# Kernel tuning notes

Hardware: AMD Instinct MI355X
Metric: run time of the kernel (lower is better)

The kernel has to match this reference:

```python
import jax, jax.numpy as jnp
import numpy as np
import math

D_MODEL = 1024
N_HEADS = 16
BATCH = 2
SEQ = 2048

def setup_inputs() -> dict:
    key = jax.random.key(0)
    ks = jax.random.split(key, 5)
    d = D_MODEL
    lim_qkv = 1.0 / math.sqrt(d)
    x = jax.random.normal(ks[0], (BATCH, SEQ, d), dtype=jnp.float32)
    qkv_w = jax.random.uniform(ks[1], (3 * d, d), dtype=jnp.float32, minval=-lim_qkv, maxval=lim_qkv)
    qkv_b = jax.random.uniform(ks[2], (3 * d,), dtype=jnp.float32, minval=-lim_qkv, maxval=lim_qkv)
    out_w = jax.random.uniform(ks[3], (d, d), dtype=jnp.float32, minval=-lim_qkv, maxval=lim_qkv)
    out_b = jax.random.uniform(ks[4], (d,), dtype=jnp.float32, minval=-lim_qkv, maxval=lim_qkv)
    return {"x": x, "qkv_w": qkv_w, "qkv_b": qkv_b, "out_w": out_w, "out_b": out_b}

def reference(x, qkv_w, qkv_b, out_w, out_b):
    b, s, d = x.shape
    h = N_HEADS
    hd = d // h
    # note: original uses float division for scale: sqrt(in_features / n_heads)
    scale = math.sqrt(d / h)
    qkv = x @ qkv_w.T + qkv_b                      # [b, s, 3d]
    q, k, v = jnp.split(qkv, 3, axis=-1)           # each [b, s, d]
    def heads(t):
        return t.reshape(b, s, h, hd).transpose(0, 2, 1, 3)  # [b, h, s, hd]
    qh, kh, vh = heads(q), heads(k), heads(v)
    # faithful quirk: scores = k @ q^T (k as query, q as key)
    scores = jnp.einsum('bhid,bhjd->bhij', kh, qh) / scale   # [b, h, s, s]
    alpha = jax.nn.softmax(scores, axis=-1)
    attn = jnp.einsum('bhij,bhjd->bhid', alpha, vh)          # [b, h, s, hd]
    attn = attn.transpose(0, 2, 1, 3).reshape(b, s, d)       # [b, s, d]
    return attn @ out_w.T + out_b
```

## Files before the change

kernel.cpp:

```cpp
#include <hip/hip_runtime.h>
#include <hip/hip_fp16.h>

#define D_MODEL 1024
#define N_HEADS 16
#define HEAD_DIM 64
#define BATCH 2
#define SEQ 2048
#define ROWS (BATCH*SEQ)

#define K_SCALE 0.18033688011112042f

using h8v = __attribute__((ext_vector_type(8))) _Float16;
using h4v = __attribute__((ext_vector_type(4))) _Float16;
using g2v = __attribute__((ext_vector_type(2))) __fp16;
using g4v = __attribute__((ext_vector_type(4))) __fp16;
using f4v = __attribute__((ext_vector_type(4))) float;

__device__ __forceinline__ ushort f2h_u(float x) { return __half_as_ushort(__float2half(x)); }
__device__ __forceinline__ void splith(float x, ushort& h, ushort& l) {
    __half hh_ = __float2half(x);
    h = __half_as_ushort(hh_);
    l = f2h_u(x - __half2float(hh_));
}

__device__ __forceinline__ size_t fidx(int row, int k) {
    return ((size_t)((row >> 7) * 32 + (k >> 5)) << 12)
         + (size_t)(((row & 127) >> 4) << 9)
         + (size_t)(((row & 15) * 4 + ((k & 31) >> 3)) << 3) + (k & 7);
}

__device__ __forceinline__ void async_lds16(const ushort* g, ushort* l) {
    __builtin_amdgcn_global_load_lds(
        (const __attribute__((address_space(1))) unsigned int*)g,
        (__attribute__((address_space(3))) unsigned int*)l, 16, 0, 0);
}

__global__ __launch_bounds__(256)
void prep_kernel(const float* __restrict__ x, const float* __restrict__ qw,
                 const float* __restrict__ ow,
                 ushort* __restrict__ xh, ushort* __restrict__ qwh,
                 ushort* __restrict__ owh, ushort* __restrict__ owl)
{
    const int b = blockIdx.x, t = threadIdx.x;
    if (b < 4096) {
        const int i = b * 256 + t;
        const int row = i >> 8, k4 = (i & 255) * 4;
        const float4 v = ((const float4*)x)[i];
        ushort4 h;
        h.x = f2h_u(v.x); h.y = f2h_u(v.y); h.z = f2h_u(v.z); h.w = f2h_u(v.w);
        *(ushort4*)&xh[fidx(row, k4)] = h;
    } else if (b < 7168) {
        const int i = (b - 4096) * 256 + t;
        const int row = i >> 8, k4 = (i & 255) * 4;
        const float4 v = ((const float4*)qw)[i];
        ushort4 h;
        h.x = f2h_u(v.x); h.y = f2h_u(v.y); h.z = f2h_u(v.z); h.w = f2h_u(v.w);
        *(ushort4*)&qwh[fidx(row, k4)] = h;
    } else {
        const int i = (b - 7168) * 256 + t;
        const int row = i >> 8, k4 = (i & 255) * 4;
        const float4 v = ((const float4*)ow)[i];
        const size_t o = fidx(row, k4);
        ushort4 h, l;
        splith(v.x, h.x, l.x); splith(v.y, h.y, l.y);
        splith(v.z, h.z, l.z); splith(v.w, h.w, l.w);
        *(ushort4*)&owh[o] = h; *(ushort4*)&owl[o] = l;
    }
}

__global__ __launch_bounds__(256, 5)
void gemm_qkv(const ushort* __restrict__ Af, const ushort* __restrict__ Wf,
              const float* __restrict__ bias,
              ushort* __restrict__ Qh, ushort* __restrict__ Kh,
              ushort* __restrict__ Vt)
{
    __shared__ ushort sA[2][4096], sW[2][2048];
    const int t = threadIdx.x, lane = t & 63, wv = t >> 6;
    const int tx = lane & 15, g = lane >> 4;
    const int lin = blockIdx.x;
    const int xcd = lin & 7, r = lin >> 3;
    const int mb = xcd * 4 + (r & 3);
    const int nb = r >> 2;
    const int at0 = (wv >> 1) * 4, wt0 = (wv & 1) * 2;
    const int fo = (tx * 4 + g) * 8;
    const size_t wbase = ((size_t)(nb & 1)) << 11;

    f4v acc[8];
#pragma unroll
    for (int i = 0; i < 8; i++)
#pragma unroll
        for (int e = 0; e < 4; e++) acc[i][e] = 0.f;

    {
        const size_t ao = ((size_t)(mb * 32)) << 12;
        const size_t wo = (((size_t)((nb >> 1) * 32)) << 12) + wbase;
#pragma unroll
        for (int c = 0; c < 2; c++) {
            const int o = (t + c * 256) * 8;
            async_lds16(Af + ao + o, &sA[0][o]);
        }
        async_lds16(Wf + wo + t * 8, &sW[0][t * 8]);
    }

    for (int kt = 0; kt < 32; kt++) {
        const int p = kt & 1;
        __syncthreads();
        if (kt < 31) {
            const size_t ao = ((size_t)(mb * 32 + kt + 1)) << 12;
            const size_t wo = (((size_t)((nb >> 1) * 32 + kt + 1)) << 12) + wbase;
#pragma unroll
            for (int c = 0; c < 2; c++) {
                const int o = (t + c * 256) * 8;
                async_lds16(Af + ao + o, &sA[p ^ 1][o]);
            }
            async_lds16(Wf + wo + t * 8, &sW[p ^ 1][t * 8]);
        }
        h8v ah[4], wh[2];
#pragma unroll
        for (int i = 0; i < 4; i++)
            ah[i] = *(const h8v*)&sA[p][(at0 + i) * 512 + fo];
#pragma unroll
        for (int i = 0; i < 2; i++)
            wh[i] = *(const h8v*)&sW[p][(wt0 + i) * 512 + fo];
        if (nb < 32) {
#pragma unroll
            for (int wi = 0; wi < 2; wi++)
#pragma unroll
                for (int ai = 0; ai < 4; ai++)
                    acc[wi * 4 + ai] = __builtin_amdgcn_mfma_f32_16x16x32_f16(wh[wi], ah[ai], acc[wi * 4 + ai], 0, 0, 0);
        } else {
#pragma unroll
            for (int ai = 0; ai < 4; ai++)
#pragma unroll
                for (int wi = 0; wi < 2; wi++)
                    acc[ai * 2 + wi] = __builtin_amdgcn_mfma_f32_16x16x32_f16(ah[ai], wh[wi], acc[ai * 2 + wi], 0, 0, 0);
        }
    }

    if (nb < 32) {
        const int part = nb >> 4;
        ushort* dst = part ? Kh : Qh;
        const float scale = part ? K_SCALE : 1.0f;
#pragma unroll
        for (int wi = 0; wi < 2; wi++) {
            const int gf0 = nb * 64 + (wv & 1) * 32 + wi * 16 + g * 4;
            const float4 bv = *(const float4*)&bias[gf0];
            const int gfl = gf0 & 1023;
            const int hh = gfl >> 6;
            const int dd = gfl & 63;
#pragma unroll
            for (int ai = 0; ai < 4; ai++) {
                const int s = mb * 128 + (wv >> 1) * 64 + ai * 16 + tx;
                const int bb = s >> 11, srel = s & 2047;
                const size_t idx = (size_t)(bb * N_HEADS + hh) * 131072
                    + (size_t)(srel >> 4) * 1024 + (size_t)(dd >> 5) * 512
                    + ((srel & 15) * 4 + ((dd & 31) >> 3)) * 8 + (dd & 7);
                const f4v a = acc[wi * 4 + ai];
                ushort4 h4;
                h4.x = f2h_u((a[0] + bv.x) * scale);
                h4.y = f2h_u((a[1] + bv.y) * scale);
                h4.z = f2h_u((a[2] + bv.z) * scale);
                h4.w = f2h_u((a[3] + bv.w) * scale);
                *(ushort4*)&dst[idx] = h4;
            }
        }
    } else {
#pragma unroll
        for (int wi = 0; wi < 2; wi++) {
            const int gf = nb * 64 + (wv & 1) * 32 + wi * 16 + tx;
            const float bv = bias[gf];
            const int gfl = gf & 1023;
            const int hh = gfl >> 6;
            const int dl = gfl & 63;
#pragma unroll
            for (int ai = 0; ai < 4; ai++) {
                const int jt0 = mb * 128 + (wv >> 1) * 64 + ai * 16 + g * 4;
                const int bb = jt0 >> 11, jr = jt0 & 2047;
                const size_t idx = (size_t)(bb * N_HEADS + hh) * 131072
                    + (size_t)(jr >> 6) * 4096
                    + (size_t)((((jr >> 4) & 3) * 4) + (dl >> 4)) * 256
                    + (((jr >> 2) & 3) * 16 + (dl & 15)) * 4;
                const f4v a = acc[ai * 2 + wi];
                ushort4 h4;
                h4.x = f2h_u(a[0] + bv);
                h4.y = f2h_u(a[1] + bv);
                h4.z = f2h_u(a[2] + bv);
                h4.w = f2h_u(a[3] + bv);
                *(ushort4*)&Vt[idx] = h4;
            }
        }
    }
}

__global__ __launch_bounds__(256)
void attn_mfma(const ushort* __restrict__ Kf, const ushort* __restrict__ Qf,
               const ushort* __restrict__ Vf,
               ushort* __restrict__ Oh, ushort* __restrict__ Ol)
{
    __shared__ ushort lds[16384];
    ushort* K0 = lds + 8192;

    const int t = threadIdx.x, lane = t & 63, wv = t >> 6;
    const int tx = lane & 15, g = lane >> 4;
    const int lin = blockIdx.x;
    const int xcd = lin & 7, ix = lin >> 3;
    const int bh = xcd * 4 + (ix >> 4);
    const int it = ix & 15;
    const int b = bh >> 4, h = bh & 15;
    const int i0 = it * 128;
    const size_t hb = (size_t)bh * 131072;

    {
        const size_t kb = hb + (size_t)it * 8192;
#pragma unroll
        for (int c = 0; c < 4; c++) {
            const int o = (t + c * 256) * 8;
            async_lds16(Kf + kb + o, K0 + o);
        }
#pragma unroll
        for (int c = 0; c < 2; c++) {
            const int o = (t + c * 256) * 8;
            async_lds16(Qf + hb + o, lds + o);
            async_lds16(Vf + hb + o, lds + 4096 + o);
        }
    }
    __syncthreads();

    const int fo = (tx * 4 + g) * 8;
    h8v kf[2][2];
#pragma unroll
    for (int is = 0; is < 2; is++)
#pragma unroll
        for (int kk = 0; kk < 2; kk++)
            kf[is][kk] = *(const h8v*)&K0[((wv * 2 + is) * 2 + kk) * 512 + fo];

    f4v O[2][4];
    float l_acc[2] = {0.f, 0.f};
#pragma unroll
    for (int is = 0; is < 2; is++)
#pragma unroll
        for (int ht = 0; ht < 4; ht++)
#pragma unroll
            for (int e = 0; e < 4; e++) O[is][ht][e] = 0.f;

    for (int jt = 0; jt < SEQ / 64; jt++) {
        ushort* buf = lds + (jt & 1) * 8192;
        ushort* nxt = lds + ((jt & 1) ^ 1) * 8192;
        __syncthreads();
        if (jt < SEQ / 64 - 1) {
            const size_t off = hb + (size_t)(jt + 1) * 4096;
#pragma unroll
            for (int c = 0; c < 2; c++) {
                const int o = (t + c * 256) * 8;
                async_lds16(Qf + off + o, nxt + o);
                async_lds16(Vf + off + o, nxt + 4096 + o);
            }
        }
        const ushort* sQ = buf;
        const ushort* sV = buf + 4096;

        f4v sc[2][4];
#pragma unroll
        for (int is = 0; is < 2; is++)
#pragma unroll
            for (int jn = 0; jn < 4; jn++)
#pragma unroll
                for (int e = 0; e < 4; e++) sc[is][jn][e] = 0.f;
#pragma unroll
        for (int kk = 0; kk < 2; kk++)
#pragma unroll
            for (int jn = 0; jn < 4; jn++) {
                const h8v qf = *(const h8v*)&sQ[(jn * 2 + kk) * 512 + fo];
#pragma unroll
                for (int is = 0; is < 2; is++)
                    sc[is][jn] = __builtin_amdgcn_mfma_f32_16x16x32_f16(qf, kf[is][kk], sc[is][jn], 0, 0, 0);
            }

        h4v ph[2][4];
#pragma unroll
        for (int is = 0; is < 2; is++)
#pragma unroll
            for (int jn = 0; jn < 4; jn++) {
                const float p0 = __builtin_amdgcn_exp2f(sc[is][jn][0]);
                const float p1 = __builtin_amdgcn_exp2f(sc[is][jn][1]);
                const float p2 = __builtin_amdgcn_exp2f(sc[is][jn][2]);
                const float p3 = __builtin_amdgcn_exp2f(sc[is][jn][3]);
                l_acc[is] += (p0 + p1) + (p2 + p3);
                const g2v plo = __builtin_amdgcn_cvt_pkrtz(p0, p1);
                const g2v phi = __builtin_amdgcn_cvt_pkrtz(p2, p3);
                const g4v pk = __builtin_shufflevector(plo, phi, 0, 1, 2, 3);
                ph[is][jn] = __builtin_bit_cast(h4v, pk);
            }

#pragma unroll
        for (int jc = 0; jc < 4; jc++)
#pragma unroll
            for (int ht = 0; ht < 4; ht++) {
                const h4v vf = *(const h4v*)&sV[(jc * 4 + ht) * 256 + (g * 16 + tx) * 4];
#pragma unroll
                for (int is = 0; is < 2; is++)
                    O[is][ht] = __builtin_amdgcn_mfma_f32_16x16x16f16(vf, ph[is][jc], O[is][ht], 0, 0, 0);
            }
    }

#pragma unroll
    for (int is = 0; is < 2; is++) {
        float l = l_acc[is];
        l += __shfl_xor(l, 16);
        l += __shfl_xor(l, 32);
        const float inv = 1.0f / l;
        const int row = b * SEQ + i0 + (wv * 2 + is) * 16 + tx;
#pragma unroll
        for (int ht = 0; ht < 4; ht++) {
            const int k0 = h * 64 + ht * 16 + g * 4;
            const size_t o = fidx(row, k0);
            ushort4 hv, lv;
            float v;
            v = O[is][ht][0] * inv; splith(v, hv.x, lv.x);
            v = O[is][ht][1] * inv; splith(v, hv.y, lv.y);
            v = O[is][ht][2] * inv; splith(v, hv.z, lv.z);
            v = O[is][ht][3] * inv; splith(v, hv.w, lv.w);
            *(ushort4*)&Oh[o] = hv;
            *(ushort4*)&Ol[o] = lv;
        }
    }
}

__global__ __launch_bounds__(256, 4)
void gemm_out(const ushort* __restrict__ Af, const ushort* __restrict__ Alf,
              const ushort* __restrict__ Wf, const ushort* __restrict__ Wlf,
              const float* __restrict__ bias, float* __restrict__ out)
{
    __shared__ ushort sA[2][4096], sW[2][4096];
    const int t = threadIdx.x, lane = t & 63, wv = t >> 6;
    const int tx = lane & 15, g = lane >> 4;
    const int lin = blockIdx.x;
    const int xcd = lin & 7, r = lin >> 3;
    const int nb = xcd * 2 + (r & 1);
    const int mb = r >> 1;
    const int at0 = (wv >> 1) * 2, wt0 = (wv & 1) * 2;
    const int fo = (tx * 4 + g) * 8;
    const size_t abase = ((size_t)(mb & 1)) << 11;
    const size_t wbase = ((size_t)(nb & 1)) << 11;

    f4v acc[4];
#pragma unroll
    for (int i = 0; i < 4; i++)
#pragma unroll
        for (int e = 0; e < 4; e++) acc[i][e] = 0.f;

    {
        const size_t ao = (((size_t)((mb >> 1) * 32)) << 12) + abase;
        const size_t wo = (((size_t)((nb >> 1) * 32)) << 12) + wbase;
        const int o = t * 8;
        async_lds16(Af + ao + o, &sA[0][o]);
        async_lds16(Alf + ao + o, &sA[0][2048 + o]);
        async_lds16(Wf + wo + o, &sW[0][o]);
        async_lds16(Wlf + wo + o, &sW[0][2048 + o]);
    }

    for (int kt = 0; kt < 32; kt++) {
        const int p = kt & 1;
        __syncthreads();
        if (kt < 31) {
            const size_t ao = (((size_t)((mb >> 1) * 32 + kt + 1)) << 12) + abase;
            const size_t wo = (((size_t)((nb >> 1) * 32 + kt + 1)) << 12) + wbase;
            const int o = t * 8;
            async_lds16(Af + ao + o, &sA[p ^ 1][o]);
            async_lds16(Alf + ao + o, &sA[p ^ 1][2048 + o]);
            async_lds16(Wf + wo + o, &sW[p ^ 1][o]);
            async_lds16(Wlf + wo + o, &sW[p ^ 1][2048 + o]);
        }
        h8v ah[2], al[2], wh[2], wl[2];
#pragma unroll
        for (int i = 0; i < 2; i++) {
            ah[i] = *(const h8v*)&sA[p][(at0 + i) * 512 + fo];
            al[i] = *(const h8v*)&sA[p][2048 + (at0 + i) * 512 + fo];
            wh[i] = *(const h8v*)&sW[p][(wt0 + i) * 512 + fo];
            wl[i] = *(const h8v*)&sW[p][2048 + (wt0 + i) * 512 + fo];
        }
#pragma unroll
        for (int wi = 0; wi < 2; wi++)
#pragma unroll
            for (int ai = 0; ai < 2; ai++) {
                acc[wi * 2 + ai] = __builtin_amdgcn_mfma_f32_16x16x32_f16(wh[wi], ah[ai], acc[wi * 2 + ai], 0, 0, 0);
                acc[wi * 2 + ai] = __builtin_amdgcn_mfma_f32_16x16x32_f16(wh[wi], al[ai], acc[wi * 2 + ai], 0, 0, 0);
                acc[wi * 2 + ai] = __builtin_amdgcn_mfma_f32_16x16x32_f16(wl[wi], ah[ai], acc[wi * 2 + ai], 0, 0, 0);
            }
    }

#pragma unroll
    for (int wi = 0; wi < 2; wi++) {
        const int gf0 = nb * 64 + (wv & 1) * 32 + wi * 16 + g * 4;
        const float4 bv = *(const float4*)&bias[gf0];
#pragma unroll
        for (int ai = 0; ai < 2; ai++) {
            const int tok = mb * 64 + (wv >> 1) * 32 + ai * 16 + tx;
            const f4v a = acc[wi * 2 + ai];
            float4 o;
            o.x = a[0] + bv.x;
            o.y = a[1] + bv.y;
            o.z = a[2] + bv.z;
            o.w = a[3] + bv.w;
            *(float4*)&out[(size_t)tok * D_MODEL + gf0] = o;
        }
    }
}

extern "C" void kernel_launch(void* const* d_in, const int* in_sizes, int n_in,
                              void* d_out, int out_size, void* d_ws, size_t ws_size,
                              hipStream_t stream) {
    const float* x     = (const float*)d_in[0];
    const float* qkv_w = (const float*)d_in[1];
    const float* qkv_b = (const float*)d_in[2];
    const float* out_w = (const float*)d_in[3];
    const float* out_b = (const float*)d_in[4];
    float* out = (float*)d_out;

    const size_t FB = (size_t)ROWS * D_MODEL;
    const size_t MM = (size_t)D_MODEL * D_MODEL;
    ushort* u   = (ushort*)d_ws;
    ushort* xh  = u;
    ushort* Ol  = u + FB;
    ushort* Qh  = u + 2 * FB;
    ushort* Kh  = u + 3 * FB;
    ushort* Vt  = u + 4 * FB;
    ushort* qwh = u + 5 * FB;
    ushort* owh = u + 5 * FB + 3 * MM;
    ushort* owl = owh + MM;

    prep_kernel<<<8192, 256, 0, stream>>>(x, qkv_w, out_w, xh, qwh, owh, owl);
    gemm_qkv<<<1536, 256, 0, stream>>>(xh, qwh, qkv_b, Qh, Kh, Vt);
    attn_mfma<<<512, 256, 0, stream>>>(Kh, Qh, Vt, xh, Ol);
    gemm_out<<<1024, 256, 0, stream>>>(xh, Ol, owh, owl, out_b, out);
}
```

Baseline: 215.4 us.

## Software-pipeline attention loop with triple buffering and 16x16x32 PV MFMA

Restructures the attention inner loop so the PV MFMAs for the previous tile run alongside the QK scores for the current tile, and the exp2 softmax step for the current tile comes after them. Q/V tiles are triple-buffered in a larger LDS allocation to make this possible. The V layout written by the QKV projection is also changed so PV can use 16x16x32 MFMA with 8-wide fragments, halving the number of PV MFMA instructions. The cost is more LDS per block (64KB), which may reduce occupancy, and extra live registers for the carried probabilities.

```diff
diff --git a/kernel.cpp b/kernel.cpp
--- a/kernel.cpp
+++ b/kernel.cpp
@@ -176,10 +176,14 @@
             for (int ai = 0; ai < 4; ai++) {
                 const int jt0 = mb * 128 + (wv >> 1) * 64 + ai * 16 + g * 4;
                 const int bb = jt0 >> 11, jr = jt0 & 2047;
+                const int jj = jr & 63;
                 const size_t idx = (size_t)(bb * N_HEADS + hh) * 131072
                     + (size_t)(jr >> 6) * 4096
-                    + (size_t)((((jr >> 4) & 3) * 4) + (dl >> 4)) * 256
-                    + (((jr >> 2) & 3) * 16 + (dl & 15)) * 4;
+                    + (size_t)(jj >> 5) * 2048
+                    + (size_t)((dl >> 4) & 3) * 512
+                    + (size_t)((jj >> 2) & 3) * 128
+                    + (size_t)(dl & 15) * 8
+                    + (size_t)((jj >> 4) & 1) * 4;
                 const f4v a = acc[ai * 2 + wi];
                 ushort4 h4;
                 h4.x = f2h_u(a[0] + bv);
@@ -197,8 +201,9 @@
                const ushort* __restrict__ Vf,
                ushort* __restrict__ Oh, ushort* __restrict__ Ol)
 {
-    __shared__ ushort lds[16384];
-    ushort* K0 = lds + 8192;
+    __shared__ ushort lds[32768];
+    ushort* KR = lds;
+    ushort* bufs = lds + 8192;
 
     const int t = threadIdx.x, lane = t & 63, wv = t >> 6;
     const int tx = lane & 15, g = lane >> 4;
@@ -215,24 +220,35 @@
 #pragma unroll
         for (int c = 0; c < 4; c++) {
             const int o = (t + c * 256) * 8;
-            async_lds16(Kf + kb + o, K0 + o);
+            async_lds16(Kf + kb + o, KR + o);
         }
 #pragma unroll
         for (int c = 0; c < 2; c++) {
             const int o = (t + c * 256) * 8;
-            async_lds16(Qf + hb + o, lds + o);
-            async_lds16(Vf + hb + o, lds + 4096 + o);
+            async_lds16(Qf + hb + o, bufs + o);
+            async_lds16(Vf + hb + o, bufs + 4096 + o);
         }
     }
     __syncthreads();
 
     const int fo = (tx * 4 + g) * 8;
+    const int vo = (g * 16 + tx) * 8;
     h8v kf[2][2];
 #pragma unroll
     for (int is = 0; is < 2; is++)
 #pragma unroll
         for (int kk = 0; kk < 2; kk++)
-            kf[is][kk] = *(const h8v*)&K0[((wv * 2 + is) * 2 + kk) * 512 + fo];
+            kf[is][kk] = *(const h8v*)&KR[((wv * 2 + is) * 2 + kk) * 512 + fo];
+
+    {
+        const size_t off = hb + 4096;
+#pragma unroll
+        for (int c = 0; c < 2; c++) {
+            const int o = (t + c * 256) * 8;
+            async_lds16(Qf + off + o, bufs + 8192 + o);
+            async_lds16(Vf + off + o, bufs + 8192 + 4096 + o);
+        }
+    }
 
     f4v O[2][4];
     float l_acc[2] = {0.f, 0.f};
@@ -243,22 +259,10 @@
 #pragma unroll
             for (int e = 0; e < 4; e++) O[is][ht][e] = 0.f;
 
-    for (int jt = 0; jt < SEQ / 64; jt++) {
-        ushort* buf = lds + (jt & 1) * 8192;
-        ushort* nxt = lds + ((jt & 1) ^ 1) * 8192;
-        __syncthreads();
-        if (jt < SEQ / 64 - 1) {
-            const size_t off = hb + (size_t)(jt + 1) * 4096;
-#pragma unroll
-            for (int c = 0; c < 2; c++) {
-                const int o = (t + c * 256) * 8;
-                async_lds16(Qf + off + o, nxt + o);
-                async_lds16(Vf + off + o, nxt + 4096 + o);
-            }
-        }
-        const ushort* sQ = buf;
-        const ushort* sV = buf + 4096;
-
+    h4v php[2][4];
+
+    {
+        const ushort* sQ = bufs;
         f4v sc[2][4];
 #pragma unroll
         for (int is = 0; is < 2; is++)
@@ -275,8 +279,6 @@
                 for (int is = 0; is < 2; is++)
                     sc[is][jn] = __builtin_amdgcn_mfma_f32_16x16x32_f16(qf, kf[is][kk], sc[is][jn], 0, 0, 0);
             }
-
-        h4v ph[2][4];
 #pragma unroll
         for (int is = 0; is < 2; is++)
 #pragma unroll
@@ -289,18 +291,93 @@
                 const g2v plo = __builtin_amdgcn_cvt_pkrtz(p0, p1);
                 const g2v phi = __builtin_amdgcn_cvt_pkrtz(p2, p3);
                 const g4v pk = __builtin_shufflevector(plo, phi, 0, 1, 2, 3);
-                ph[is][jn] = __builtin_bit_cast(h4v, pk);
-            }
-
-#pragma unroll
-        for (int jc = 0; jc < 4; jc++)
+                php[is][jn] = __builtin_bit_cast(h4v, pk);
+            }
+    }
+
+    int bp = 0, bc = 1, bn = 2;
+    for (int jt = 1; jt < SEQ / 64; jt++) {
+        __syncthreads();
+        if (jt < SEQ / 64 - 1) {
+            const size_t off = hb + (size_t)(jt + 1) * 4096;
+#pragma unroll
+            for (int c = 0; c < 2; c++) {
+                const int o = (t + c * 256) * 8;
+                async_lds16(Qf + off + o, bufs + bn * 8192 + o);
+                async_lds16(Vf + off + o, bufs + bn * 8192 + 4096 + o);
+            }
+        }
+        const ushort* sQ = bufs + bc * 8192;
+        const ushort* sVp = bufs + bp * 8192 + 4096;
+
+        f4v sc[2][4];
+#pragma unroll
+        for (int is = 0; is < 2; is++)
+#pragma unroll
+            for (int jn = 0; jn < 4; jn++)
+#pragma unroll
+                for (int e = 0; e < 4; e++) sc[is][jn][e] = 0.f;
+#pragma unroll
+        for (int kk = 0; kk < 2; kk++)
+#pragma unroll
+            for (int jn = 0; jn < 4; jn++) {
+                const h8v qf = *(const h8v*)&sQ[(jn * 2 + kk) * 512 + fo];
+#pragma unroll
+                for (int is = 0; is < 2; is++)
+                    sc[is][jn] = __builtin_amdgcn_mfma_f32_16x16x32_f16(qf, kf[is][kk], sc[is][jn], 0, 0, 0);
+            }
+
+#pragma unroll
+        for (int jc = 0; jc < 2; jc++) {
+            h8v p8[2];
+#pragma unroll
+            for (int is = 0; is < 2; is++)
+                p8[is] = __builtin_shufflevector(php[is][jc * 2], php[is][jc * 2 + 1],
+                                                 0, 1, 2, 3, 4, 5, 6, 7);
 #pragma unroll
             for (int ht = 0; ht < 4; ht++) {
-                const h4v vf = *(const h4v*)&sV[(jc * 4 + ht) * 256 + (g * 16 + tx) * 4];
+                const h8v vf = *(const h8v*)&sVp[jc * 2048 + ht * 512 + vo];
 #pragma unroll
                 for (int is = 0; is < 2; is++)
-                    O[is][ht] = __builtin_amdgcn_mfma_f32_16x16x16f16(vf, ph[is][jc], O[is][ht], 0, 0, 0);
-            }
+                    O[is][ht] = __builtin_amdgcn_mfma_f32_16x16x32_f16(vf, p8[is], O[is][ht], 0, 0, 0);
+            }
+        }
+
+#pragma unroll
+        for (int is = 0; is < 2; is++)
+#pragma unroll
+            for (int jn = 0; jn < 4; jn++) {
+                const float p0 = __builtin_amdgcn_exp2f(sc[is][jn][0]);
+                const float p1 = __builtin_amdgcn_exp2f(sc[is][jn][1]);
+                const float p2 = __builtin_amdgcn_exp2f(sc[is][jn][2]);
+                const float p3 = __builtin_amdgcn_exp2f(sc[is][jn][3]);
+                l_acc[is] += (p0 + p1) + (p2 + p3);
+                const g2v plo = __builtin_amdgcn_cvt_pkrtz(p0, p1);
+                const g2v phi = __builtin_amdgcn_cvt_pkrtz(p2, p3);
+                const g4v pk = __builtin_shufflevector(plo, phi, 0, 1, 2, 3);
+                php[is][jn] = __builtin_bit_cast(h4v, pk);
+            }
+
+        const int tmp = bp; bp = bc; bc = bn; bn = tmp;
+    }
+
+    {
+        const ushort* sVp = bufs + bp * 8192 + 4096;
+#pragma unroll
+        for (int jc = 0; jc < 2; jc++) {
+            h8v p8[2];
+#pragma unroll
+            for (int is = 0; is < 2; is++)
+                p8[is] = __builtin_shufflevector(php[is][jc * 2], php[is][jc * 2 + 1],
+                                                 0, 1, 2, 3, 4, 5, 6, 7);
+#pragma unroll
+            for (int ht = 0; ht < 4; ht++) {
+                const h8v vf = *(const h8v*)&sVp[jc * 2048 + ht * 512 + vo];
+#pragma unroll
+                for (int is = 0; is < 2; is++)
+                    O[is][ht] = __builtin_amdgcn_mfma_f32_16x16x32_f16(vf, p8[is], O[is][ht], 0, 0, 0);
+            }
+        }
     }
 
 #pragma unroll
```

After: 207.2 us. -3.8%, faster.

## Stream Q/V tiles from global into registers, use K=32 MFMA for PV

Applied to the files above, without the earlier changes.

The attention kernel no longer stages Q and V tiles through double-buffered LDS with block-wide barriers. Each wave now loads its fragments straight from global memory into registers, ping-ponging two register sets so the next tile's loads overlap the current compute. The PV product switches from 16x16x16 to 16x16x32 MFMA by packing pairs of probability fragments, and the V projection epilogue writes a new layout with 8-wide stores to match. It also adds s_setprio around the MFMA blocks and launch bounds of 2 blocks per SM, at the cost of more register pressure and redundant global reads across waves.

```diff
diff --git a/kernel.cpp b/kernel.cpp
--- a/kernel.cpp
+++ b/kernel.cpp
@@ -14,6 +14,7 @@
 using h4v = __attribute__((ext_vector_type(4))) _Float16;
 using g2v = __attribute__((ext_vector_type(2))) __fp16;
 using g4v = __attribute__((ext_vector_type(4))) __fp16;
+using us8 = __attribute__((ext_vector_type(8))) unsigned short;
 using f4v = __attribute__((ext_vector_type(4))) float;
 
 __device__ __forceinline__ ushort f2h_u(float x) { return __half_as_ushort(__float2half(x)); }
@@ -172,33 +173,33 @@
             const int gfl = gf & 1023;
             const int hh = gfl >> 6;
             const int dl = gfl & 63;
-#pragma unroll
-            for (int ai = 0; ai < 4; ai++) {
-                const int jt0 = mb * 128 + (wv >> 1) * 64 + ai * 16 + g * 4;
-                const int bb = jt0 >> 11, jr = jt0 & 2047;
-                const size_t idx = (size_t)(bb * N_HEADS + hh) * 131072
-                    + (size_t)(jr >> 6) * 4096
-                    + (size_t)((((jr >> 4) & 3) * 4) + (dl >> 4)) * 256
-                    + (((jr >> 2) & 3) * 16 + (dl & 15)) * 4;
-                const f4v a = acc[ai * 2 + wi];
-                ushort4 h4;
-                h4.x = f2h_u(a[0] + bv);
-                h4.y = f2h_u(a[1] + bv);
-                h4.z = f2h_u(a[2] + bv);
-                h4.w = f2h_u(a[3] + bv);
-                *(ushort4*)&Vt[idx] = h4;
+            const int t0 = mb * 2 + (wv >> 1);
+            const int bb = t0 >> 5;
+            const size_t base = (size_t)(bb * N_HEADS + hh) * 131072
+                + (size_t)(t0 & 31) * 4096
+                + (size_t)((dl >> 4) & 3) * 512
+                + (size_t)g * 128 + (size_t)(dl & 15) * 8;
+#pragma unroll
+            for (int aip = 0; aip < 2; aip++) {
+                const f4v a0 = acc[(2 * aip) * 2 + wi];
+                const f4v a1 = acc[(2 * aip + 1) * 2 + wi];
+                us8 s;
+                s[0] = f2h_u(a0[0] + bv); s[1] = f2h_u(a0[1] + bv);
+                s[2] = f2h_u(a0[2] + bv); s[3] = f2h_u(a0[3] + bv);
+                s[4] = f2h_u(a1[0] + bv); s[5] = f2h_u(a1[1] + bv);
+                s[6] = f2h_u(a1[2] + bv); s[7] = f2h_u(a1[3] + bv);
+                *(us8*)&Vt[base + (size_t)aip * 2048] = s;
             }
         }
     }
 }
 
-__global__ __launch_bounds__(256)
+__global__ __launch_bounds__(256, 2)
 void attn_mfma(const ushort* __restrict__ Kf, const ushort* __restrict__ Qf,
                const ushort* __restrict__ Vf,
                ushort* __restrict__ Oh, ushort* __restrict__ Ol)
 {
-    __shared__ ushort lds[16384];
-    ushort* K0 = lds + 8192;
+    __shared__ ushort KR[8192];
 
     const int t = threadIdx.x, lane = t & 63, wv = t >> 6;
     const int tx = lane & 15, g = lane >> 4;
@@ -215,24 +216,22 @@
 #pragma unroll
         for (int c = 0; c < 4; c++) {
             const int o = (t + c * 256) * 8;
-            async_lds16(Kf + kb + o, K0 + o);
-        }
-#pragma unroll
-        for (int c = 0; c < 2; c++) {
-            const int o = (t + c * 256) * 8;
-            async_lds16(Qf + hb + o, lds + o);
-            async_lds16(Vf + hb + o, lds + 4096 + o);
+            async_lds16(Kf + kb + o, KR + o);
         }
     }
     __syncthreads();
 
     const int fo = (tx * 4 + g) * 8;
+    const int vo = (g * 16 + tx) * 8;
     h8v kf[2][2];
 #pragma unroll
     for (int is = 0; is < 2; is++)
 #pragma unroll
         for (int kk = 0; kk < 2; kk++)
-            kf[is][kk] = *(const h8v*)&K0[((wv * 2 + is) * 2 + kk) * 512 + fo];
+            kf[is][kk] = *(const h8v*)&KR[((wv * 2 + is) * 2 + kk) * 512 + fo];
+
+    const ushort* Qb = Qf + hb;
+    const ushort* Vb = Vf + hb;
 
     f4v O[2][4];
     float l_acc[2] = {0.f, 0.f};
@@ -243,22 +242,24 @@
 #pragma unroll
             for (int e = 0; e < 4; e++) O[is][ht][e] = 0.f;
 
-    for (int jt = 0; jt < SEQ / 64; jt++) {
-        ushort* buf = lds + (jt & 1) * 8192;
-        ushort* nxt = lds + ((jt & 1) ^ 1) * 8192;
-        __syncthreads();
-        if (jt < SEQ / 64 - 1) {
-            const size_t off = hb + (size_t)(jt + 1) * 4096;
-#pragma unroll
-            for (int c = 0; c < 2; c++) {
-                const int o = (t + c * 256) * 8;
-                async_lds16(Qf + off + o, nxt + o);
-                async_lds16(Vf + off + o, nxt + 4096 + o);
-            }
-        }
-        const ushort* sQ = buf;
-        const ushort* sV = buf + 4096;
-
+    auto loadQ = [&](h8v (&q)[2][4], int jt) {
+        const ushort* qp = Qb + (size_t)jt * 4096;
+#pragma unroll
+        for (int kk = 0; kk < 2; kk++)
+#pragma unroll
+            for (int jn = 0; jn < 4; jn++)
+                q[kk][jn] = *(const h8v*)&qp[(jn * 2 + kk) * 512 + fo];
+    };
+    auto loadV = [&](h8v (&v)[2][4], int jt) {
+        const ushort* vp = Vb + (size_t)jt * 4096;
+#pragma unroll
+        for (int jc = 0; jc < 2; jc++)
+#pragma unroll
+            for (int ht = 0; ht < 4; ht++)
+                v[jc][ht] = *(const h8v*)&vp[jc * 2048 + ht * 512 + vo];
+    };
+
+    auto compute = [&](const h8v (&q)[2][4], const h8v (&v)[2][4]) {
         f4v sc[2][4];
 #pragma unroll
         for (int is = 0; is < 2; is++)
@@ -266,17 +267,17 @@
             for (int jn = 0; jn < 4; jn++)
 #pragma unroll
                 for (int e = 0; e < 4; e++) sc[is][jn][e] = 0.f;
+        __builtin_amdgcn_s_setprio(1);
 #pragma unroll
         for (int kk = 0; kk < 2; kk++)
 #pragma unroll
-            for (int jn = 0; jn < 4; jn++) {
-                const h8v qf = *(const h8v*)&sQ[(jn * 2 + kk) * 512 + fo];
+            for (int jn = 0; jn < 4; jn++)
 #pragma unroll
                 for (int is = 0; is < 2; is++)
-                    sc[is][jn] = __builtin_amdgcn_mfma_f32_16x16x32_f16(qf, kf[is][kk], sc[is][jn], 0, 0, 0);
-            }
-
-        h4v ph[2][4];
+                    sc[is][jn] = __builtin_amdgcn_mfma_f32_16x16x32_f16(q[kk][jn], kf[is][kk], sc[is][jn], 0, 0, 0);
+        __builtin_amdgcn_s_setprio(0);
+
+        h4v php[2][4];
 #pragma unroll
         for (int is = 0; is < 2; is++)
 #pragma unroll
@@ -289,18 +290,33 @@
                 const g2v plo = __builtin_amdgcn_cvt_pkrtz(p0, p1);
                 const g2v phi = __builtin_amdgcn_cvt_pkrtz(p2, p3);
                 const g4v pk = __builtin_shufflevector(plo, phi, 0, 1, 2, 3);
-                ph[is][jn] = __builtin_bit_cast(h4v, pk);
+                php[is][jn] = __builtin_bit_cast(h4v, pk);
             }
 
-#pragma unroll
-        for (int jc = 0; jc < 4; jc++)
-#pragma unroll
-            for (int ht = 0; ht < 4; ht++) {
-                const h4v vf = *(const h4v*)&sV[(jc * 4 + ht) * 256 + (g * 16 + tx) * 4];
+        __builtin_amdgcn_s_setprio(1);
+#pragma unroll
+        for (int jc = 0; jc < 2; jc++) {
+            h8v p8[2];
+#pragma unroll
+            for (int is = 0; is < 2; is++)
+                p8[is] = __builtin_shufflevector(php[is][jc * 2], php[is][jc * 2 + 1],
+                                                 0, 1, 2, 3, 4, 5, 6, 7);
+#pragma unroll
+            for (int ht = 0; ht < 4; ht++)
 #pragma unroll
                 for (int is = 0; is < 2; is++)
-                    O[is][ht] = __builtin_amdgcn_mfma_f32_16x16x16f16(vf, ph[is][jc], O[is][ht], 0, 0, 0);
-            }
+                    O[is][ht] = __builtin_amdgcn_mfma_f32_16x16x32_f16(v[jc][ht], p8[is], O[is][ht], 0, 0, 0);
+        }
+        __builtin_amdgcn_s_setprio(0);
+    };
+
+    h8v qA[2][4], vA[2][4], qB[2][4], vB[2][4];
+    loadQ(qA, 0); loadV(vA, 0);
+    for (int jt = 0; jt < SEQ / 64; jt += 2) {
+        loadQ(qB, jt + 1); loadV(vB, jt + 1);
+        compute(qA, vA);
+        if (jt + 2 < SEQ / 64) { loadQ(qA, jt + 2); loadV(vA, jt + 2); }
+        compute(qB, vB);
     }
 
 #pragma unroll
```

Result: faster. 208.4 us (-3.2%).
